# Optimization experiments

Hardware: AMD Instinct MI355X
Metric: run time of the kernel (lower is better)

## Reference

```python
import jax, jax.numpy as jnp
import numpy as np

K = 1024          # num_embeddings
D = 64            # embedding_dim
TEMP = 1.0        # cfg.temperature
EPS = 1e-10


def setup_inputs() -> dict:
    key = jax.random.key(0)
    k1, k2 = jax.random.split(key)
    return {
        "inputs": jax.random.normal(k1, (16, 2048, D), dtype=jnp.float32),
        "embedding": jax.random.normal(k2, (K, D), dtype=jnp.float32),
        "code_count": jnp.ones((K,), dtype=jnp.float32),
    }


def _distances(flat, embedding):
    return ((flat ** 2).sum(axis=1, keepdims=True)
            + (embedding ** 2).sum(axis=1)
            - 2.0 * flat @ embedding.T)


def reference(inputs, embedding, code_count):
    B = inputs.shape[0]
    flat = inputs.reshape(-1, D)                      # [N, D]
    N = flat.shape[0]

    d = _distances(flat, embedding)                   # [N, K]
    idx = jnp.argmin(d, axis=1)                       # [N]

    # one-hot @ codebook == gather by index
    quantized = embedding[idx].reshape(inputs.shape)

    commitment_loss = jnp.mean((jax.lax.stop_gradient(quantized) - inputs) ** 2)

    # ortho loss over used codes (code_count >= 1), via masking (jit-safe)
    mask = (code_count >= 1.0).astype(inputs.dtype)   # [K]
    n_used = mask.sum()
    normed = embedding / jnp.clip(
        jnp.linalg.norm(embedding, axis=1, keepdims=True), 1e-12)
    normed = normed * mask[:, None]                   # zero out unused rows
    cos = normed @ normed.T                           # [K, K]
    ortho_loss = (cos ** 2).sum() / (n_used ** 2) - 1.0 / n_used

    # entropy loss over softmax(-d / T)
    prob = jax.nn.softmax(-d / TEMP, axis=1)          # [N, K]
    entropy_loss = -jnp.mean(jnp.sum(prob * jnp.log(prob + EPS), axis=1))
    entropy_loss = entropy_loss / jnp.log2(jnp.asarray(K, inputs.dtype))

    # straight-through estimator
    quantized_st = inputs + jax.lax.stop_gradient(quantized - inputs)

    # perplexity from code usage histogram (mean of one-hot encodings)
    avg_probs = jnp.zeros((K,), inputs.dtype).at[idx].add(1.0) / N
    perplexity = jnp.exp(-jnp.sum(avg_probs * jnp.log(avg_probs + EPS)))

    coverage = mask.sum() / K
    indices = idx.reshape(B, -1)

    return (quantized_st, commitment_loss, ortho_loss, entropy_loss,
            perplexity, coverage, indices)
```

## Files before the change

kernel.cpp:

```cpp
#include <hip/hip_runtime.h>
#include <math.h>

#define N_ROWS  32768
#define K_CODES 1024
#define D_DIM   64
#define NSPLIT  4
#define C_SHIFT 30.0f
#define LOG2E_F 1.4426950408889634f
#define LN2_F   0.6931471805599453f
#define TAU     0.25f

#define WS_E2C    6144
#define PART_STRIDE (NSPLIT * N_ROWS)
#define WS_PART_S  8192
#define WS_PART_U  (8192 + PART_STRIDE)
#define WS_PART_M1 (8192 + 2 * PART_STRIDE)
#define WS_PART_M2 (8192 + 3 * PART_STRIDE)
#define CHUNK_F4  260
#define MAIN_CHUNKS 16
#define WS_EB      (8192 + 4 * PART_STRIDE)
#define WS_GP      (WS_EB + 64 * CHUNK_F4 * 4)
#define WS_HB      (WS_GP + 16 * 4096)
#define WS_PH      (WS_HB + 16 * K_CODES)
#define WS_PC      (WS_PH + 512)

#define OUT_Q      0
#define OUT_COMMIT 2097152
#define OUT_ORTHO  2097153
#define OUT_ENT    2097154
#define OUT_PERP   2097155
#define OUT_COV    2097156
#define OUT_IDX    2097157

typedef __attribute__((ext_vector_type(8))) _Float16 f16x8;
typedef __attribute__((ext_vector_type(4))) float f32x4;

__device__ inline unsigned umaxu(unsigned a, unsigned b) { return a > b ? a : b; }
__device__ inline unsigned uminu(unsigned a, unsigned b) { return a < b ? a : b; }

__device__ inline float keyval(unsigned u) {
    unsigned b = (u & 0x80000000u) ? (u ^ 0x80000000u) : ~u;
    return __uint_as_float(b);
}

__device__ inline void decomp2x8(const float* v, f16x8& h, f16x8& m) {
#pragma unroll
    for (int i = 0; i < 8; ++i) {
        _Float16 hh = (_Float16)v[i];
        h[i] = hh;
        m[i] = (_Float16)(v[i] - (float)hh);
    }
}

__global__ __launch_bounds__(256) void vq_prep_ortho(const float* __restrict__ emb,
                                                     const float* __restrict__ cc,
                                                     float* __restrict__ ws) {
    __shared__ float srows[64][64];
    __shared__ float rn2[64];
    const int t = threadIdx.x;

    if (blockIdx.x < 16) {
        const int tid  = blockIdx.x * 256 + t;
        const int c    = tid >> 6;
        const int lane = tid & 63;
        const int col  = lane & 15;
        const int kg   = lane >> 4;
        const int code = c * 16 + col;
        float4* EB4 = (float4*)(ws + WS_EB);
#pragma unroll
        for (int s = 0; s < 2; ++s) {
            const float* ep = emb + (size_t)code * D_DIM + s * 32 + kg * 8;
            float4 A4 = *(const float4*)ep;
            float4 B4 = *(const float4*)(ep + 4);
            float v[8] = {A4.x, A4.y, A4.z, A4.w, B4.x, B4.y, B4.z, B4.w};
            union { f16x8 h; float4 f; } th, tm;
            decomp2x8(v, th.h, tm.h);
            const int base = c * CHUNK_F4;
            EB4[base + (s * 2 + 0) * 64 + lane] = th.f;
            EB4[base + (s * 2 + 1) * 64 + lane] = tm.f;
        }
        if (kg == 0) {
            const float4* e4 = (const float4*)(emb + (size_t)code * D_DIM);
            float ssum = 0.f;
#pragma unroll
            for (int j = 0; j < 16; ++j) {
                float4 v = e4[j];
                ssum += v.x * v.x + v.y * v.y + v.z * v.z + v.w * v.w;
            }
            float e2c = ssum + C_SHIFT;
            ws[WS_E2C + code] = e2c;
            ((float*)(EB4 + c * CHUNK_F4 + 256))[col] = e2c * LOG2E_F;
        }
        return;
    }

    const int ob = blockIdx.x - 16;
    const int k0 = ob * 64;
    const int rb = t >> 4;
    const int c4 = (t & 15) << 2;

#pragma unroll
    for (int i = 0; i < 4; ++i) {
        const int r = i * 16 + rb;
        float4 v = *(const float4*)(emb + (size_t)(k0 + r) * D_DIM + c4);
        *(float4*)(&srows[r][c4]) = v;
        float ss = v.x * v.x + v.y * v.y + v.z * v.z + v.w * v.w;
        ss += __shfl_down(ss, 8, 16);
        ss += __shfl_down(ss, 4, 16);
        ss += __shfl_down(ss, 2, 16);
        ss += __shfl_down(ss, 1, 16);
        if ((t & 15) == 0) {
            float nrm = fmaxf(sqrtf(ss), 1e-12f);
            float m = (cc[k0 + r] >= 1.0f) ? 1.0f : 0.0f;
            rn2[r] = m / (nrm * nrm);
        }
    }
    __syncthreads();

    const int a  = t >> 2;
    const int b0 = (t & 3) << 4;
    float acc[16];
#pragma unroll
    for (int i = 0; i < 16; ++i) acc[i] = 0.f;

#pragma unroll 4
    for (int k = 0; k < 64; ++k) {
        float na = srows[k][a] * rn2[k];
        const float* rbp = &srows[k][b0];
#pragma unroll
        for (int i = 0; i < 16; ++i) acc[i] = fmaf(na, rbp[i], acc[i]);
    }
#pragma unroll
    for (int i = 0; i < 16; ++i)
        ws[WS_GP + ob * 4096 + a * 64 + b0 + i] = acc[i];
}

#define MFMA_F16 __builtin_amdgcn_mfma_f32_16x16x32_f16

__global__ __launch_bounds__(256)
void vq_main(const float* __restrict__ inp, float* __restrict__ ws) {
    const int t    = threadIdx.x;
    const int lane = t & 63;
    const int wave = t >> 6;
    const int col  = lane & 15;
    const int kg   = lane >> 4;
    const int rg   = blockIdx.x >> 2;
    const int sp   = blockIdx.x & 3;
    const int row  = rg * 64 + wave * 16 + col;

    f16x8 xh0, xm0, xh1, xm1;
    {
        const float* xp = inp + (size_t)row * D_DIM + kg * 8;
        float4 A4 = *(const float4*)xp;
        float4 B4 = *(const float4*)(xp + 4);
        float v[8] = {A4.x, A4.y, A4.z, A4.w, B4.x, B4.y, B4.z, B4.w};
        decomp2x8(v, xh0, xm0);
        A4 = *(const float4*)(xp + 32);
        B4 = *(const float4*)(xp + 36);
        float w[8] = {A4.x, A4.y, A4.z, A4.w, B4.x, B4.y, B4.z, B4.w};
        decomp2x8(w, xh1, xm1);
    }

    const float4* EBp = (const float4*)(ws + WS_EB)
                      + (size_t)sp * MAIN_CHUNKS * CHUNK_F4;

    float sa[4], ua[4];
    unsigned m1[4], m2[4];
#pragma unroll
    for (int q = 0; q < 4; ++q) {
        sa[q] = 0.f; ua[q] = 0.f;
        m1[q] = 0u; m2[q] = 0u;
    }

#pragma unroll 1
    for (int c = 0; c < MAIN_CHUNKS; ++c) {
        const float4* p = EBp + (size_t)c * CHUNK_F4;
        const f16x8* pb = (const f16x8*)p;
        f16x8 bh0 = pb[0 * 64 + lane];
        f16x8 bm0 = pb[1 * 64 + lane];
        f16x8 bh1 = pb[2 * 64 + lane];
        f16x8 bm1 = pb[3 * 64 + lane];
        const float e2v = ((const float*)(p + 256))[col];

        f32x4 acc = {0.f, 0.f, 0.f, 0.f};
        acc = MFMA_F16(xh0, bh0, acc, 0, 0, 0);
        acc = MFMA_F16(xh1, bh1, acc, 0, 0, 0);
        acc = MFMA_F16(xm0, bh0, acc, 0, 0, 0);
        acc = MFMA_F16(xm1, bh1, acc, 0, 0, 0);
        acc = MFMA_F16(xh0, bm0, acc, 0, 0, 0);
        acc = MFMA_F16(xh1, bm1, acc, 0, 0, 0);
        acc = MFMA_F16(xm0, bm0, acc, 0, 0, 0);
        acc = MFMA_F16(xm1, bm1, acc, 0, 0, 0);

        const unsigned embedv = 255u - (unsigned)(c * 16 + col);
#pragma unroll
        for (int q = 0; q < 4; ++q) {
            float g = fmaf(2.0f * LOG2E_F, acc[q], -e2v);
            float pw;
            asm("v_exp_f32 %0, %1" : "=v"(pw) : "v"(g));
            sa[q] += pw;
            ua[q] = fmaf(pw, g, ua[q]);
            int gb = __float_as_int(g);
            unsigned u = (unsigned)(gb ^ ((gb >> 31) | 0x80000000));
            unsigned key = (u & 0xFFFFFF00u) | embedv;
            m2[q] = uminu(umaxu(key, m2[q]), m1[q]);
            m1[q] = umaxu(m1[q], key);
        }
    }

#pragma unroll
    for (int off = 1; off < 16; off <<= 1) {
#pragma unroll
        for (int q = 0; q < 4; ++q) {
            sa[q] += __shfl_xor(sa[q], off);
            ua[q] += __shfl_xor(ua[q], off);
            unsigned p1 = (unsigned)__shfl_xor((int)m1[q], off);
            unsigned p2 = (unsigned)__shfl_xor((int)m2[q], off);
            unsigned lo = uminu(m1[q], p1);
            m1[q] = umaxu(m1[q], p1);
            m2[q] = umaxu(lo, umaxu(m2[q], p2));
        }
    }

    if (col == 0) {
#pragma unroll
        for (int q = 0; q < 4; ++q) {
            const int r  = rg * 64 + wave * 16 + kg * 4 + q;
            const int pi = sp * N_ROWS + r;
            ws[WS_PART_S  + pi] = sa[q];
            ws[WS_PART_U  + pi] = ua[q];
            ws[WS_PART_M1 + pi] = __uint_as_float(m1[q]);
            ws[WS_PART_M2 + pi] = __uint_as_float(m2[q]);
        }
    }
}

__global__ __launch_bounds__(256) void vq_combine(const float* __restrict__ inp,
                                                  const float* __restrict__ emb,
                                                  float* __restrict__ ws,
                                                  float* __restrict__ out) {
    __shared__ float shH[4], shC[4];
    const int t    = threadIdx.x;
    const int lane = t & 63;
    const int wave = t >> 6;
    const int l    = t & 3;
    const int row  = blockIdx.x * 64 + (t >> 2);
    const int qb   = lane & ~3;

    const int pi = l * N_ROWS + row;
    float    Sl = ws[WS_PART_S  + pi];
    float    Ul = ws[WS_PART_U  + pi];
    unsigned K1 = __float_as_uint(ws[WS_PART_M1 + pi]);
    unsigned K2 = __float_as_uint(ws[WS_PART_M2 + pi]);
    float    G1 = keyval(K1);

    float S = 0.f, U2 = 0.f, Gmax = -1e30f;
#pragma unroll
    for (int k = 0; k < 4; ++k) {
        S  += __shfl(Sl, qb + k);
        U2 += __shfl(Ul, qb + k);
        Gmax = fmaxf(Gmax, __shfl(G1, qb + k));
    }

    float4 Xq[4];
    const float4* xr = (const float4*)(inp + (size_t)row * D_DIM);
#pragma unroll
    for (int k = 0; k < 4; ++k) Xq[k] = xr[l + 4 * k];

    float bestg = -1e30f; int I = K_CODES;
#pragma unroll 1
    for (int j = 0; j < 8; ++j) {
        const int sp = j >> 1;
        const unsigned kk = (unsigned)__shfl((int)((j & 1) ? K2 : K1), qb + sp);
        const float v = keyval(kk);
        if (v < Gmax - TAU) continue;
        const int c = sp * 256 + 255 - (int)(kk & 255u);
        const float4* e4 = (const float4*)(emb + (size_t)c * D_DIM);
        float d = 0.f;
#pragma unroll
        for (int k = 0; k < 4; ++k) {
            float4 ev = e4[l + 4 * k];
            float4 xv = Xq[k];
            d = fmaf(ev.x, xv.x, d); d = fmaf(ev.y, xv.y, d);
            d = fmaf(ev.z, xv.z, d); d = fmaf(ev.w, xv.w, d);
        }
        float dA = __shfl(d, qb + 0) + __shfl(d, qb + 1);
        float dB = __shfl(d, qb + 2) + __shfl(d, qb + 3);
        float g  = fmaf(2.0f, dA + dB, -ws[WS_E2C + c]);
        if (g > bestg || (g == bestg && c < I)) { bestg = g; I = c; }
    }

    float H = logf(S) - (U2 * LN2_F) / S;

    if (l == 0) out[OUT_IDX + row] = (float)I;

    const float4* q4 = (const float4*)(emb + (size_t)I * D_DIM);
    float4* oq = (float4*)out + (size_t)row * 16;
    float cs = 0.f;
#pragma unroll
    for (int k = 0; k < 4; ++k) {
        float4 q = q4[l + 4 * k], x = Xq[k];
        float dx = q.x - x.x, dy = q.y - x.y, dz = q.z - x.z, dw = q.w - x.w;
        cs += dx * dx + dy * dy + dz * dz + dw * dw;
        float4 o;
        o.x = x.x + dx; o.y = x.y + dy; o.z = x.z + dz; o.w = x.w + dw;
        oq[l + 4 * k] = o;
    }

    float Hc = (l == 0) ? H : 0.f;
#pragma unroll
    for (int off = 32; off; off >>= 1) {
        Hc += __shfl_down(Hc, off);
        cs += __shfl_down(cs, off);
    }
    if (lane == 0) { shH[wave] = Hc; shC[wave] = cs; }
    __syncthreads();
    if (t == 0) {
        ws[WS_PH + blockIdx.x] = shH[0] + shH[1] + shH[2] + shH[3];
        ws[WS_PC + blockIdx.x] = shC[0] + shC[1] + shC[2] + shC[3];
    }
}

__global__ __launch_bounds__(256) void vq_hist(const float* __restrict__ out,
                                               float* __restrict__ ws) {
    __shared__ int h[K_CODES];
    const int t = threadIdx.x;
#pragma unroll
    for (int i = 0; i < 4; ++i) h[t + 256 * i] = 0;
    __syncthreads();
    const int base = blockIdx.x * 2048;
#pragma unroll
    for (int i = 0; i < 8; ++i) {
        int idx = (int)out[OUT_IDX + base + t + 256 * i];
        atomicAdd(&h[idx], 1);
    }
    __syncthreads();
#pragma unroll
    for (int i = 0; i < 4; ++i) {
        const int k = t + 256 * i;
        ws[WS_HB + blockIdx.x * K_CODES + k] = (float)h[k];
    }
}

__global__ __launch_bounds__(256) void vq_finalize(const float* __restrict__ ws,
                                                   const float* __restrict__ cc,
                                                   float* __restrict__ out) {
    __shared__ float red[5][4];
    const int t = threadIdx.x;
    float hp = 0.f, gg = 0.f, nu = 0.f, hh = 0.f, cm = 0.f;
    for (int k = t; k < K_CODES; k += 256) {
        float s = 0.f;
#pragma unroll
        for (int b = 0; b < 16; ++b) s += ws[WS_HB + b * K_CODES + k];
        float p = s * (1.0f / (float)N_ROWS);
        hp += p * logf(p + 1e-10f);
        nu += (cc[k] >= 1.0f) ? 1.0f : 0.0f;
    }
    for (int i = t; i < 4096; i += 256) {
        float s = 0.f;
#pragma unroll
        for (int b = 0; b < 16; ++b) s += ws[WS_GP + b * 4096 + i];
        gg = fmaf(s, s, gg);
    }
    for (int i = t; i < 512; i += 256) {
        hh += ws[WS_PH + i];
        cm += ws[WS_PC + i];
    }
#pragma unroll
    for (int off = 32; off; off >>= 1) {
        hp += __shfl_down(hp, off);
        gg += __shfl_down(gg, off);
        nu += __shfl_down(nu, off);
        hh += __shfl_down(hh, off);
        cm += __shfl_down(cm, off);
    }
    if ((t & 63) == 0) {
        const int w = t >> 6;
        red[0][w] = hp; red[1][w] = gg; red[2][w] = nu;
        red[3][w] = hh; red[4][w] = cm;
    }
    __syncthreads();
    if (t == 0) {
        float hsum = red[0][0] + red[0][1] + red[0][2] + red[0][3];
        float gsum = red[1][0] + red[1][1] + red[1][2] + red[1][3];
        float nuv  = red[2][0] + red[2][1] + red[2][2] + red[2][3];
        float hacc = red[3][0] + red[3][1] + red[3][2] + red[3][3];
        float cacc = red[4][0] + red[4][1] + red[4][2] + red[4][3];
        out[OUT_PERP]   = expf(-hsum);
        out[OUT_ENT]    = hacc * (1.0f / (float)N_ROWS) * 0.1f;
        out[OUT_COMMIT] = cacc * (1.0f / ((float)N_ROWS * (float)D_DIM));
        out[OUT_ORTHO]  = gsum / (nuv * nuv) - 1.0f / nuv;
        out[OUT_COV]    = nuv * (1.0f / (float)K_CODES);
    }
}

extern "C" void kernel_launch(void* const* d_in, const int* in_sizes, int n_in,
                              void* d_out, int out_size, void* d_ws, size_t ws_size,
                              hipStream_t stream) {
    const float* inp = (const float*)d_in[0];
    const float* emb = (const float*)d_in[1];
    const float* cc  = (const float*)d_in[2];
    float* out = (float*)d_out;
    float* ws  = (float*)d_ws;

    vq_prep_ortho<<<32, 256, 0, stream>>>(emb, cc, ws);
    vq_main<<<(N_ROWS / 64) * NSPLIT, 256, 0, stream>>>(inp, ws);
    vq_combine<<<N_ROWS / 64, 256, 0, stream>>>(inp, emb, ws, out);
    vq_hist<<<16, 256, 0, stream>>>(out, ws);
    vq_finalize<<<1, 256, 0, stream>>>(ws, cc, out);
}
```

Measured before the change: 118.9 us.

## Software-pipeline codebook loads in vq_main and fuse histogram with finalize

The main distance loop is unrolled by two with double-buffered register loads, so the next chunk's codebook fragments are fetched while the MFMAs and epilogue of the current chunk run. Separately, the histogram and finalize kernels are merged into one launch: the last block to finish, found through an atomic counter reset in the prep kernel, performs the final reductions. This removes one kernel launch and hides load latency, at the cost of more live registers and a fence-plus-atomic handshake.

Measured after the change: 120.5 us. No clear change (+1.3%).

```diff
diff --git a/kernel.cpp b/kernel.cpp
--- a/kernel.cpp
+++ b/kernel.cpp
@@ -10,6 +10,7 @@
 #define LN2_F   0.6931471805599453f
 #define TAU     0.25f
 
+#define WS_CNT    0
 #define WS_E2C    6144
 #define PART_STRIDE (NSPLIT * N_ROWS)
 #define WS_PART_S  8192
@@ -60,6 +61,8 @@
     const int t = threadIdx.x;
 
     if (blockIdx.x < 16) {
+        if (blockIdx.x == 0 && t == 0) ((int*)ws)[WS_CNT] = 0;
+
         const int tid  = blockIdx.x * 256 + t;
         const int c    = tid >> 6;
         const int lane = tid & 63;
@@ -137,6 +140,32 @@
 
 #define MFMA_F16 __builtin_amdgcn_mfma_f32_16x16x32_f16
 
+#define EPI(ACC, E2V, CIDX) do {                                             \
+    const unsigned embedv = 255u - (unsigned)((CIDX) * 16 + col);            \
+    _Pragma("unroll")                                                        \
+    for (int q = 0; q < 4; ++q) {                                            \
+        float g = fmaf(2.0f * LOG2E_F, (ACC)[q], -(E2V));                    \
+        float pw;                                                            \
+        asm("v_exp_f32 %0, %1" : "=v"(pw) : "v"(g));                         \
+        sa[q] += pw;                                                         \
+        ua[q] = fmaf(pw, g, ua[q]);                                          \
+        int gb = __float_as_int(g);                                          \
+        unsigned u = (unsigned)(gb ^ ((gb >> 31) | 0x80000000));             \
+        unsigned key = (u & 0xFFFFFF00u) | embedv;                           \
+        m2[q] = uminu(umaxu(key, m2[q]), m1[q]);                             \
+        m1[q] = umaxu(m1[q], key);                                           \
+    }                                                                        \
+} while (0)
+
+#define LOADF(P, F0, F1, F2, F3, E2) do {                                    \
+    const f16x8* pb_ = (const f16x8*)(P);                                    \
+    F0 = pb_[0 * 64 + lane];                                                 \
+    F1 = pb_[1 * 64 + lane];                                                 \
+    F2 = pb_[2 * 64 + lane];                                                 \
+    F3 = pb_[3 * 64 + lane];                                                 \
+    E2 = ((const float*)((P) + 256))[col];                                   \
+} while (0)
+
 __global__ __launch_bounds__(256)
 void vq_main(const float* __restrict__ inp, float* __restrict__ ws) {
     const int t    = threadIdx.x;
@@ -172,40 +201,38 @@
         m1[q] = 0u; m2[q] = 0u;
     }
 
+    f16x8 a0, a1, a2, a3, b0, b1, b2, b3;
+    float ae2, be2;
+    LOADF(EBp, a0, a1, a2, a3, ae2);
+
 #pragma unroll 1
-    for (int c = 0; c < MAIN_CHUNKS; ++c) {
-        const float4* p = EBp + (size_t)c * CHUNK_F4;
-        const f16x8* pb = (const f16x8*)p;
-        f16x8 bh0 = pb[0 * 64 + lane];
-        f16x8 bm0 = pb[1 * 64 + lane];
-        f16x8 bh1 = pb[2 * 64 + lane];
-        f16x8 bm1 = pb[3 * 64 + lane];
-        const float e2v = ((const float*)(p + 256))[col];
-
+    for (int c = 0; c < MAIN_CHUNKS; c += 2) {
         f32x4 acc = {0.f, 0.f, 0.f, 0.f};
-        acc = MFMA_F16(xh0, bh0, acc, 0, 0, 0);
-        acc = MFMA_F16(xh1, bh1, acc, 0, 0, 0);
-        acc = MFMA_F16(xm0, bh0, acc, 0, 0, 0);
-        acc = MFMA_F16(xm1, bh1, acc, 0, 0, 0);
-        acc = MFMA_F16(xh0, bm0, acc, 0, 0, 0);
-        acc = MFMA_F16(xh1, bm1, acc, 0, 0, 0);
-        acc = MFMA_F16(xm0, bm0, acc, 0, 0, 0);
-        acc = MFMA_F16(xm1, bm1, acc, 0, 0, 0);
-
-        const unsigned embedv = 255u - (unsigned)(c * 16 + col);
-#pragma unroll
-        for (int q = 0; q < 4; ++q) {
-            float g = fmaf(2.0f * LOG2E_F, acc[q], -e2v);
-            float pw;
-            asm("v_exp_f32 %0, %1" : "=v"(pw) : "v"(g));
-            sa[q] += pw;
-            ua[q] = fmaf(pw, g, ua[q]);
-            int gb = __float_as_int(g);
-            unsigned u = (unsigned)(gb ^ ((gb >> 31) | 0x80000000));
-            unsigned key = (u & 0xFFFFFF00u) | embedv;
-            m2[q] = uminu(umaxu(key, m2[q]), m1[q]);
-            m1[q] = umaxu(m1[q], key);
-        }
+        acc = MFMA_F16(xh0, a0, acc, 0, 0, 0);
+        acc = MFMA_F16(xh1, a2, acc, 0, 0, 0);
+        acc = MFMA_F16(xm0, a0, acc, 0, 0, 0);
+        acc = MFMA_F16(xm1, a2, acc, 0, 0, 0);
+        acc = MFMA_F16(xh0, a1, acc, 0, 0, 0);
+        acc = MFMA_F16(xh1, a3, acc, 0, 0, 0);
+        acc = MFMA_F16(xm0, a1, acc, 0, 0, 0);
+        acc = MFMA_F16(xm1, a3, acc, 0, 0, 0);
+        LOADF(EBp + (size_t)(c + 1) * CHUNK_F4, b0, b1, b2, b3, be2);
+        EPI(acc, ae2, c);
+
+        f32x4 acd = {0.f, 0.f, 0.f, 0.f};
+        acd = MFMA_F16(xh0, b0, acd, 0, 0, 0);
+        acd = MFMA_F16(xh1, b2, acd, 0, 0, 0);
+        acd = MFMA_F16(xm0, b0, acd, 0, 0, 0);
+        acd = MFMA_F16(xm1, b2, acd, 0, 0, 0);
+        acd = MFMA_F16(xh0, b1, acd, 0, 0, 0);
+        acd = MFMA_F16(xh1, b3, acd, 0, 0, 0);
+        acd = MFMA_F16(xm0, b1, acd, 0, 0, 0);
+        acd = MFMA_F16(xm1, b3, acd, 0, 0, 0);
+        {
+            const int cn = (c + 2 < MAIN_CHUNKS) ? c + 2 : c;
+            LOADF(EBp + (size_t)cn * CHUNK_F4, a0, a1, a2, a3, ae2);
+        }
+        EPI(acd, be2, c + 1);
     }
 
 #pragma unroll
@@ -321,9 +348,12 @@
     }
 }
 
-__global__ __launch_bounds__(256) void vq_hist(const float* __restrict__ out,
-                                               float* __restrict__ ws) {
+__global__ __launch_bounds__(256) void vq_hist_fin(const float* __restrict__ cc,
+                                                   float* __restrict__ ws,
+                                                   float* __restrict__ out) {
     __shared__ int h[K_CODES];
+    __shared__ int lastFlag;
+    __shared__ float red[5][4];
     const int t = threadIdx.x;
 #pragma unroll
     for (int i = 0; i < 4; ++i) h[t + 256 * i] = 0;
@@ -340,18 +370,24 @@
         const int k = t + 256 * i;
         ws[WS_HB + blockIdx.x * K_CODES + k] = (float)h[k];
     }
-}
-
-__global__ __launch_bounds__(256) void vq_finalize(const float* __restrict__ ws,
-                                                   const float* __restrict__ cc,
-                                                   float* __restrict__ out) {
-    __shared__ float red[5][4];
-    const int t = threadIdx.x;
+    __threadfence();
+    __syncthreads();
+    if (t == 0) {
+        int old = __hip_atomic_fetch_add((int*)ws + WS_CNT, 1,
+                                         __ATOMIC_ACQ_REL,
+                                         __HIP_MEMORY_SCOPE_AGENT);
+        lastFlag = (old == 15);
+    }
+    __syncthreads();
+    if (!lastFlag) return;
+
     float hp = 0.f, gg = 0.f, nu = 0.f, hh = 0.f, cm = 0.f;
     for (int k = t; k < K_CODES; k += 256) {
         float s = 0.f;
 #pragma unroll
-        for (int b = 0; b < 16; ++b) s += ws[WS_HB + b * K_CODES + k];
+        for (int b = 0; b < 16; ++b)
+            s += __hip_atomic_load(ws + WS_HB + b * K_CODES + k,
+                                   __ATOMIC_RELAXED, __HIP_MEMORY_SCOPE_AGENT);
         float p = s * (1.0f / (float)N_ROWS);
         hp += p * logf(p + 1e-10f);
         nu += (cc[k] >= 1.0f) ? 1.0f : 0.0f;
@@ -406,6 +442,5 @@
     vq_prep_ortho<<<32, 256, 0, stream>>>(emb, cc, ws);
     vq_main<<<(N_ROWS / 64) * NSPLIT, 256, 0, stream>>>(inp, ws);
     vq_combine<<<N_ROWS / 64, 256, 0, stream>>>(inp, emb, ws, out);
-    vq_hist<<<16, 256, 0, stream>>>(out, ws);
-    vq_finalize<<<1, 256, 0, stream>>>(ws, cc, out);
-}
+    vq_hist_fin<<<16, 256, 0, stream>>>(cc, ws, out);
+}
```
